# Kernel tuning notes

Measured on AMD Instinct MI355X. Metric: run time of the kernel, lower is better.

The kernel has to match this reference:

```python
import jax, jax.numpy as jnp
import numpy as np

SCALE = 32.0      # backbone feature->image coordinate scale (stride)
LOG_EPS = 1e-8    # geometry.safe_log epsilon


def _safe_log(x):
    return jnp.log(jnp.maximum(x, LOG_EPS))


def setup_inputs() -> dict:
    key = jax.random.key(0)
    k1, k2, k3, k4, k5, k6 = jax.random.split(key, 6)
    B, P, L = 128, 4096, 128
    cls_scores = jax.random.normal(k1, (B, 2 * P), dtype=jnp.float32)
    bbox_deltas = jax.random.normal(k2, (B, 4 * P), dtype=jnp.float32) * 0.1
    # RoI in feature coordinates: x,y in [0,40), w,h in [1,11)
    roi_xy = jax.random.uniform(k3, (B, P, 2), dtype=jnp.float32) * 40.0
    roi_wh = jax.random.uniform(k4, (B, P, 2), dtype=jnp.float32) * 10.0 + 1.0
    roi = jnp.concatenate([roi_xy, roi_wh], axis=-1)
    # Ground-truth labels in image coordinates: x,y in [0,1280), w,h in [32,352)
    lab_xy = jax.random.uniform(k5, (B, L, 2), dtype=jnp.float32) * 1280.0
    lab_wh = jax.random.uniform(k6, (B, L, 2), dtype=jnp.float32) * 320.0 + 32.0
    labels = jnp.concatenate([lab_xy, lab_wh], axis=-1)
    return {
        "cls_scores": cls_scores,
        "bbox_deltas": bbox_deltas,
        "roi": roi,
        "labels": labels,
        "neg_enabled": 1,
    }


def reference(cls_scores, bbox_deltas, roi, labels, neg_enabled):
    """Vectorized port of ClassifierModel._compute_loss summed over the batch.

    cls_scores  [B, 2P] laid out [class, proposal] (cls[i::P] -> per-proposal logits)
    bbox_deltas [B, 4P] laid out [coord, proposal]
    roi         [B, P, 4] proposals in feature coords (x,y,w,h)
    labels      [B, L, 4] ground-truth boxes in image coords (x,y,w,h)
    """
    B, P = roi.shape[0], roi.shape[1]
    roi_img = roi.astype(jnp.float32) * SCALE  # feature -> image coords

    # --- IoU matrix [B, L, P] (geometry.calculate_IoU over all label/proposal pairs)
    l = labels[:, :, None, :]   # [B, L, 1, 4]
    r = roi_img[:, None, :, :]  # [B, 1, P, 4]
    ix = jnp.maximum(0.0, jnp.minimum(l[..., 0] + l[..., 2], r[..., 0] + r[..., 2]) - jnp.maximum(l[..., 0], r[..., 0]))
    iy = jnp.maximum(0.0, jnp.minimum(l[..., 1] + l[..., 3], r[..., 1] + r[..., 3]) - jnp.maximum(l[..., 1], r[..., 1]))
    inter = ix * iy
    union = l[..., 2] * l[..., 3] + r[..., 2] * r[..., 3] - inter
    iou = jnp.where(union > 0.0, inter / union, 0.0)  # [B, L, P]

    # --- matching: argmax over labels where any IoU is nonzero, else -1
    any_hit = jnp.sum((iou != 0.0).astype(jnp.int32), axis=1) > 0        # [B, P]
    match = jnp.where(any_hit, jnp.argmax(iou, axis=1), -1)              # [B, P]
    pos = match > 0  # NOTE: original uses match[i] > 0 (strict), kept faithfully

    matched = jnp.take_along_axis(labels, jnp.clip(match, 0)[:, :, None], axis=1)  # [B, P, 4]
    tx = (matched[..., 0] - roi_img[..., 0]) / roi_img[..., 2]
    ty = (matched[..., 1] - roi_img[..., 1]) / roi_img[..., 3]
    tw = _safe_log(matched[..., 2] / roi_img[..., 2])
    th = _safe_log(matched[..., 3] / roi_img[..., 3])
    targets = jnp.stack([tx, ty, tw, th], axis=-1)                        # [B, P, 4]
    preds = bbox_deltas.reshape(B, 4, P).transpose(0, 2, 1)               # [B, P, 4]

    # Huber (delta=1, mean over the 4 coords) per proposal
    err = targets - preds
    ae = jnp.abs(err)
    huber = jnp.mean(jnp.where(ae <= 1.0, 0.5 * err * err, ae - 0.5), axis=-1)  # [B, P]

    # --- classification: softmax over the two per-proposal logits, then
    # CategoricalCrossentropy(probs, const) = -sum(probs * log(const))
    logits = cls_scores.reshape(B, 2, P).transpose(0, 2, 1)               # [B, P, 2]
    probs = jax.nn.softmax(logits, axis=-1)
    log_pos = jnp.log(jnp.array([0.1, 0.9], dtype=jnp.float32))
    log_neg = jnp.log(jnp.array([0.9, 0.1], dtype=jnp.float32))
    ce_pos = -jnp.sum(probs * log_pos, axis=-1)                           # [B, P]
    ce_neg = -jnp.sum(probs * log_neg, axis=-1)                           # [B, P]

    neg_term = jnp.where(jnp.asarray(neg_enabled) > 0, ce_neg, 0.0)
    per_prop = jnp.where(pos, 2.0 * huber + ce_pos, neg_term)             # [B, P]
    return jnp.sum(per_prop)
```

## Files before the change

### kernel.cpp

```cpp
#include <hip/hip_runtime.h>
#include <hip/hip_bf16.h>
#include <math.h>

#define BB 128
#define PP 4096
#define LL 128
#define BLOCK 256
#define PROPS 2
#define CHUNKS (PP / (BLOCK * PROPS))
#define SCALE 32.0f
#define LCHUNK 8

__global__ __launch_bounds__(BLOCK) void classifier_loss_kernel(
    const float* __restrict__ cls,
    const float* __restrict__ bbox,
    const float* __restrict__ roi,
    const float* __restrict__ labels,
    const int* __restrict__ neg_enabled,
    float* __restrict__ out)
{
    __shared__ float4 s_lab4[LL];
    __shared__ float  s_red[BLOCK / 64];

    const int b     = blockIdx.x >> 3;
    const int chunk = blockIdx.x & (CHUNKS - 1);
    const int pbase = chunk * (BLOCK * PROPS) + threadIdx.x;

    if (threadIdx.x < LL) {
        const float* lp = labels + ((size_t)b * LL + threadIdx.x) * 4;
        float x = lp[0], y = lp[1], w = lp[2], h = lp[3];
        s_lab4[threadIdx.x] = make_float4(x, y, x + w, y + h);
    }

    float rx[PROPS], ry[PROPS], rx2[PROPS], ry2[PROPS], rarea[PROPS];
    float cs0[PROPS], cs1[PROPS];
    float best[PROPS];

    #pragma unroll
    for (int j = 0; j < PROPS; ++j) {
        const int p = pbase + j * BLOCK;
        const float* rp = roi + ((size_t)b * PP + p) * 4;
        float r0 = rp[0], r1 = rp[1], r2 = rp[2], r3 = rp[3];
        cs0[j] = cls[(size_t)b * 2 * PP + p];
        cs1[j] = cls[(size_t)b * 2 * PP + PP + p];
        rx[j]  = r0 * SCALE;
        ry[j]  = r1 * SCALE;
        float rw = r2 * SCALE, rh = r3 * SCALE;
        rx2[j] = rx[j] + rw;
        ry2[j] = ry[j] + rh;
        rarea[j] = rw * rh;
        best[j] = 0.0f;
    }

    __syncthreads();

    for (int lc = 0; lc < LL; lc += LCHUNK) {
        #pragma unroll
        for (int u = 0; u < LCHUNK; ++u) {
            const int li = lc + u;
            const float4 l4 = s_lab4[li];
            const float S = (l4.z - l4.x) * (l4.w - l4.y);
            #pragma unroll
            for (int j = 0; j < PROPS; ++j) {
                float ix = fmaxf(0.0f, fminf(l4.z, rx2[j]) - fmaxf(l4.x, rx[j]));
                float iy = fminf(l4.w, ry2[j]) - fmaxf(l4.y, ry[j]);
                float inter = ix * iy;
                float denom = S + rarea[j];
                float c = inter * __builtin_amdgcn_rcpf(denom);
                unsigned kb = (__float_as_uint(c) & 0xFFFFFF80u) | (unsigned)(127 - li);
                best[j] = fmaxf(best[j], __uint_as_float(kb));
            }
        }
    }

    const float LOG01 = -2.3025850929940457f;
    const float LOG09 = -0.10536051565782628f;
    const bool neg_on = neg_enabled[0] > 0;

    float acc = 0.0f;
    #pragma unroll
    for (int j = 0; j < PROPS; ++j) {
        const int p = pbase + j * BLOCK;
        const int bidx = 127 - (int)(__float_as_uint(best[j]) & 127u);
        const bool pos = (best[j] > 1e-25f) && (bidx > 0);

        const float mx = fmaxf(cs0[j], cs1[j]);
        const float e0 = expf(cs0[j] - mx);
        const float e1 = expf(cs1[j] - mx);
        const float inv = 1.0f / (e0 + e1);
        const float p0 = e0 * inv, p1 = e1 * inv;
        const float ce_pos = -(p0 * LOG01 + p1 * LOG09);
        const float ce_neg = -(p0 * LOG09 + p1 * LOG01);

        float per;
        if (pos) {
            const float* mp = labels + ((size_t)b * LL + bidx) * 4;
            float mxl = mp[0], myl = mp[1], mwl = mp[2], mhl = mp[3];
            float rw = rx2[j] - rx[j];
            float rh = ry2[j] - ry[j];
            float tx = (mxl - rx[j]) / rw;
            float ty = (myl - ry[j]) / rh;
            float tw = logf(fmaxf(mwl / rw, 1e-8f));
            float th = logf(fmaxf(mhl / rh, 1e-8f));
            const float* bp = bbox + (size_t)b * 4 * PP + p;
            float ex = tx - bp[0];
            float ey = ty - bp[PP];
            float ew = tw - bp[2 * PP];
            float eh = th - bp[3 * PP];
            float ax = fabsf(ex), ay = fabsf(ey), aw = fabsf(ew), ah = fabsf(eh);
            float hx = (ax <= 1.0f) ? 0.5f * ex * ex : ax - 0.5f;
            float hy = (ay <= 1.0f) ? 0.5f * ey * ey : ay - 0.5f;
            float hw = (aw <= 1.0f) ? 0.5f * ew * ew : aw - 0.5f;
            float hh = (ah <= 1.0f) ? 0.5f * eh * eh : ah - 0.5f;
            float huber = 0.25f * (hx + hy + hw + hh);
            per = 2.0f * huber + ce_pos;
        } else {
            per = neg_on ? ce_neg : 0.0f;
        }
        acc += per;
    }

    float v = acc;
    #pragma unroll
    for (int off = 32; off > 0; off >>= 1)
        v += __shfl_down(v, off, 64);
    if ((threadIdx.x & 63) == 0)
        s_red[threadIdx.x >> 6] = v;
    __syncthreads();
    if (threadIdx.x == 0) {
        float blk = s_red[0] + s_red[1] + s_red[2] + s_red[3];
        atomicAdd(out, blk);
    }
}

extern "C" void kernel_launch(void* const* d_in, const int* in_sizes, int n_in,
                              void* d_out, int out_size, void* d_ws, size_t ws_size,
                              hipStream_t stream) {
    const float* cls    = (const float*)d_in[0];
    const float* bbox   = (const float*)d_in[1];
    const float* roi    = (const float*)d_in[2];
    const float* labels = (const float*)d_in[3];
    const int*   neg    = (const int*)d_in[4];
    float* out = (float*)d_out;

    hipMemsetAsync(out, 0, sizeof(float), stream);
    classifier_loss_kernel<<<dim3(BB * PP / (BLOCK * PROPS)), dim3(BLOCK), 0, stream>>>(
        cls, bbox, roi, labels, neg, out);
}
```

Before: 104.7 us.

## Double-buffer shared-memory label loads in IoU loop and vectorize RoI load

Restructures the label loop so the next group of label boxes is read from shared memory into registers while the current group is processed (ping-pong A/B register buffers), and loads each RoI as a single float4 instead of four scalar loads. The aim is to hide LDS latency behind the IoU arithmetic and cut global load instructions. It raises register use, and the compiler may already have been scheduling the LDS loads this way.

```diff
diff --git a/kernel.cpp b/kernel.cpp
--- a/kernel.cpp
+++ b/kernel.cpp
@@ -1,5 +1,4 @@
 #include <hip/hip_runtime.h>
-#include <hip/hip_bf16.h>
 #include <math.h>
 
 #define BB 128
@@ -9,7 +8,7 @@
 #define PROPS 2
 #define CHUNKS (PP / (BLOCK * PROPS))
 #define SCALE 32.0f
-#define LCHUNK 8
+#define LCHUNK 4
 
 __global__ __launch_bounds__(BLOCK) void classifier_loss_kernel(
     const float* __restrict__ cls,
@@ -39,13 +38,12 @@
     #pragma unroll
     for (int j = 0; j < PROPS; ++j) {
         const int p = pbase + j * BLOCK;
-        const float* rp = roi + ((size_t)b * PP + p) * 4;
-        float r0 = rp[0], r1 = rp[1], r2 = rp[2], r3 = rp[3];
+        const float4 r4 = *reinterpret_cast<const float4*>(roi + ((size_t)b * PP + p) * 4);
         cs0[j] = cls[(size_t)b * 2 * PP + p];
         cs1[j] = cls[(size_t)b * 2 * PP + PP + p];
-        rx[j]  = r0 * SCALE;
-        ry[j]  = r1 * SCALE;
-        float rw = r2 * SCALE, rh = r3 * SCALE;
+        rx[j]  = r4.x * SCALE;
+        ry[j]  = r4.y * SCALE;
+        float rw = r4.z * SCALE, rh = r4.w * SCALE;
         rx2[j] = rx[j] + rw;
         ry2[j] = ry[j] + rh;
         rarea[j] = rw * rh;
@@ -54,23 +52,35 @@
 
     __syncthreads();
 
-    for (int lc = 0; lc < LL; lc += LCHUNK) {
+    auto process = [&](const float4& l4, int li) {
+        const float S = (l4.z - l4.x) * (l4.w - l4.y);
         #pragma unroll
-        for (int u = 0; u < LCHUNK; ++u) {
-            const int li = lc + u;
-            const float4 l4 = s_lab4[li];
-            const float S = (l4.z - l4.x) * (l4.w - l4.y);
-            #pragma unroll
-            for (int j = 0; j < PROPS; ++j) {
-                float ix = fmaxf(0.0f, fminf(l4.z, rx2[j]) - fmaxf(l4.x, rx[j]));
-                float iy = fminf(l4.w, ry2[j]) - fmaxf(l4.y, ry[j]);
-                float inter = ix * iy;
-                float denom = S + rarea[j];
-                float c = inter * __builtin_amdgcn_rcpf(denom);
-                unsigned kb = (__float_as_uint(c) & 0xFFFFFF80u) | (unsigned)(127 - li);
-                best[j] = fmaxf(best[j], __uint_as_float(kb));
-            }
+        for (int j = 0; j < PROPS; ++j) {
+            float ix = fmaxf(0.0f, fminf(l4.z, rx2[j]) - fmaxf(l4.x, rx[j]));
+            float iy = fminf(l4.w, ry2[j]) - fmaxf(l4.y, ry[j]);
+            float inter = ix * iy;
+            float den = S + rarea[j];
+            float c = inter * __builtin_amdgcn_rcpf(den);
+            unsigned kb = (__float_as_uint(c) & 0xFFFFFF80u) | (unsigned)(127 - li);
+            best[j] = fmaxf(best[j], __uint_as_float(kb));
         }
+    };
+
+    float4 A[LCHUNK], Bv[LCHUNK];
+    #pragma unroll
+    for (int u = 0; u < LCHUNK; ++u) A[u] = s_lab4[u];
+
+    for (int k = 0; k < LL / (2 * LCHUNK); ++k) {
+        const int base = k * 2 * LCHUNK;
+        #pragma unroll
+        for (int u = 0; u < LCHUNK; ++u) Bv[u] = s_lab4[base + LCHUNK + u];
+        #pragma unroll
+        for (int u = 0; u < LCHUNK; ++u) process(A[u], base + u);
+        const int nb = (base + 2 * LCHUNK) & (LL - 1);
+        #pragma unroll
+        for (int u = 0; u < LCHUNK; ++u) A[u] = s_lab4[nb + u];
+        #pragma unroll
+        for (int u = 0; u < LCHUNK; ++u) process(Bv[u], base + LCHUNK + u);
     }
 
     const float LOG01 = -2.3025850929940457f;
```

Result: slower. 107.5 us (+2.6%).
